# Optimization experiments

Hardware: AMD Instinct MI355X
Metric: run time of the kernel (lower is better)

Reference implementation:

```python
import jax, jax.numpy as jnp
import numpy as np

E = 8        # num_experts
K = 2        # num_experts_per_tok
H = 1024     # hidden_dim
F = 2816     # intermediate_dim
R = 256      # shared-core rank
B, S = 2, 1024


def setup_inputs() -> dict:
    key = jax.random.key(0)
    ks = jax.random.split(key, 12)
    inp = {
        "hidden_states": jax.random.normal(ks[0], (B, S, H), jnp.float32),
        "gate_w": jax.random.normal(ks[1], (H, E), jnp.float32) / np.sqrt(H),
        # gate_proj: hidden -> intermediate, factored W_e = Ug[e] @ Cg @ Vg[e]
        "Ug": jax.random.normal(ks[2], (E, H, R), jnp.float32) / np.sqrt(H),
        "Cg": jax.random.normal(ks[3], (R, R), jnp.float32) / np.sqrt(R),
        "Vg": jax.random.normal(ks[4], (E, R, F), jnp.float32) / np.sqrt(R),
        # up_proj: hidden -> intermediate
        "Uu": jax.random.normal(ks[5], (E, H, R), jnp.float32) / np.sqrt(H),
        "Cu": jax.random.normal(ks[6], (R, R), jnp.float32) / np.sqrt(R),
        "Vu": jax.random.normal(ks[7], (E, R, F), jnp.float32) / np.sqrt(R),
        # down_proj: intermediate -> hidden
        "Ud": jax.random.normal(ks[8], (E, F, R), jnp.float32) / np.sqrt(F),
        "Cd": jax.random.normal(ks[9], (R, R), jnp.float32) / np.sqrt(R),
        "Vd": jax.random.normal(ks[10], (E, R, H), jnp.float32) / np.sqrt(R),
    }
    return inp


def _moe_forward(x, gate_w, Ug, Cg, Vg, Uu, Cu, Vu, Ud, Cd, Vd):
    b, s, h = x.shape
    xf = x.reshape(-1, h)                       # [T, H]
    T = xf.shape[0]
    logits = xf @ gate_w                        # [T, E]
    probs = jax.nn.softmax(logits, axis=-1)
    w, idx = jax.lax.top_k(probs, K)            # [T, K]
    w = w / jnp.sum(w, axis=-1, keepdims=True)
    # dense combine weights: combine[t, e] = sum of renormalized routing
    # weights over top-k slots routed to expert e (scatter-add in torch code)
    combine = jnp.zeros((T, E), xf.dtype).at[jnp.arange(T)[:, None], idx].add(w)
    out = jnp.zeros_like(xf)
    for e in range(E):  # fixed small expert count
        g = (xf @ Ug[e]) @ Cg @ Vg[e]           # [T, F]
        u = (xf @ Uu[e]) @ Cu @ Vu[e]           # [T, F]
        a = jax.nn.silu(g) * u
        y = (a @ Ud[e]) @ Cd @ Vd[e]            # [T, H]
        out = out + combine[:, e:e + 1] * y
    return out.reshape(b, s, h)


def reference(hidden_states, gate_w, Ug, Cg, Vg, Uu, Cu, Vu, Ud, Cd, Vd):
    return _moe_forward(hidden_states, gate_w, Ug, Cg, Vg, Uu, Cu, Vu, Ud, Cd, Vd)
```

## Files before the change

kernel.cpp:

```cpp
#include <hip/hip_runtime.h>
#include <math.h>

constexpr int cE = 8;
constexpr int cH = 1024;
constexpr int cF = 2816;
constexpr int cR = 256;
constexpr int cT = 2048;
constexpr int ROWS = cT * 2;
constexpr int LDA = 40;

using short8  = __attribute__((ext_vector_type(8))) short;
using float4v = __attribute__((ext_vector_type(4))) float;
#define MFMA16 __builtin_amdgcn_mfma_f32_16x16x32_bf16

__device__ __forceinline__ unsigned short f2bf(float f) {
  union { float f; unsigned u; } v; v.f = f;
  unsigned r = v.u + 0x7fffu + ((v.u >> 16) & 1u);
  return (unsigned short)(r >> 16);
}
__device__ __forceinline__ float bf2f(unsigned short s) {
  union { unsigned u; float f; } v; v.u = (unsigned)s << 16; return v.f;
}

__device__ __forceinline__ void store_bf8(unsigned short* dst, float4 a, float4 b) {
  union { unsigned short u[8]; uint4 v; } t;
  t.u[0] = f2bf(a.x); t.u[1] = f2bf(a.y); t.u[2] = f2bf(a.z); t.u[3] = f2bf(a.w);
  t.u[4] = f2bf(b.x); t.u[5] = f2bf(b.y); t.u[6] = f2bf(b.z); t.u[7] = f2bf(b.w);
  *reinterpret_cast<uint4*>(dst) = t.v;
}

__device__ __forceinline__ void gld16(const unsigned short* g, unsigned short* l) {
  __builtin_amdgcn_global_load_lds(
      (const __attribute__((address_space(1))) void*)g,
      (__attribute__((address_space(3))) void*)l, 16, 0, 0);
}

__device__ __forceinline__ void tconv_tile64(
    const float* __restrict__ in, unsigned short* __restrict__ out,
    int P, int Q, int e, int bx, int by, int tid, float (*tile)[65])
{
  const long es = (long)P * Q;
  in += e * es; out += e * es;
  const int c0 = bx * 64, r0 = by * 64;
  const int r = tid >> 4, c4 = (tid & 15) * 4;
#pragma unroll
  for (int p = 0; p < 4; ++p) {
    float4 v = *reinterpret_cast<const float4*>(
        in + (long)(r0 + p * 16 + r) * Q + c0 + c4);
    tile[p * 16 + r][c4 + 0] = v.x; tile[p * 16 + r][c4 + 1] = v.y;
    tile[p * 16 + r][c4 + 2] = v.z; tile[p * 16 + r][c4 + 3] = v.w;
  }
  __syncthreads();
  const int cc = tid >> 4, rr4 = (tid & 15) * 4;
#pragma unroll
  for (int p = 0; p < 4; ++p) {
    ushort4 o;
    o.x = f2bf(tile[rr4 + 0][p * 16 + cc]);
    o.y = f2bf(tile[rr4 + 1][p * 16 + cc]);
    o.z = f2bf(tile[rr4 + 2][p * 16 + cc]);
    o.w = f2bf(tile[rr4 + 3][p * 16 + cc]);
    *reinterpret_cast<ushort4*>(out + (long)(c0 + p * 16 + cc) * P + r0 + rr4) = o;
  }
}

constexpr int TCONV_BLOCKS = 4768;
constexpr int PREP1_BLOCKS = TCONV_BLOCKS + cT / 4;

__global__ __launch_bounds__(256) void k_prep1(
    const float* __restrict__ Cg, unsigned short* __restrict__ CgT,
    const float* __restrict__ Cu, unsigned short* __restrict__ CuT,
    const float* __restrict__ Vd, unsigned short* __restrict__ VdT,
    const float* __restrict__ Vg, unsigned short* __restrict__ vgT,
    const float* __restrict__ Vu, unsigned short* __restrict__ vuT,
    const float* __restrict__ Ud, unsigned short* __restrict__ udT,
    const float* __restrict__ x, const float* __restrict__ gw,
    unsigned short* __restrict__ xb, int* __restrict__ et,
    float* __restrict__ wt)
{
  __shared__ float tile[64][65];
  int b = blockIdx.x;
  const int tid = threadIdx.x;
  if (b < TCONV_BLOCKS) {
    const float* in; unsigned short* out; int P, Q;
    if (b < 16)         { in = Cg; out = CgT; P = 256;  Q = 256;  }
    else if (b < 32)    { b -= 16;    in = Cu; out = CuT; P = 256;  Q = 256;  }
    else if (b < 544)   { b -= 32;    in = Vd; out = VdT; P = 256;  Q = 1024; }
    else if (b < 1952)  { b -= 544;   in = Vg; out = vgT; P = 256;  Q = 2816; }
    else if (b < 3360)  { b -= 1952;  in = Vu; out = vuT; P = 256;  Q = 2816; }
    else                { b -= 3360;  in = Ud; out = udT; P = 2816; Q = 256;  }
    const int tpe = (P / 64) * (Q / 64);
    const int e = b / tpe, rem = b % tpe;
    const int bx = rem % (Q / 64), by = rem / (Q / 64);
    tconv_tile64(in, out, P, Q, e, bx, by, tid, tile);
    return;
  }
  const int wid = tid >> 6, lane = tid & 63;
  const int t = (b - TCONV_BLOCKS) * 4 + wid;
  const float* xr = x + (long)t * cH + lane * 16;
  float4 v0 = *reinterpret_cast<const float4*>(xr);
  float4 v1 = *reinterpret_cast<const float4*>(xr + 4);
  float4 v2 = *reinterpret_cast<const float4*>(xr + 8);
  float4 v3 = *reinterpret_cast<const float4*>(xr + 12);
  store_bf8(xb + (long)t * cH + lane * 16, v0, v1);
  store_bf8(xb + (long)t * cH + lane * 16 + 8, v2, v3);
  float xv[16];
  *reinterpret_cast<float4*>(&xv[0])  = v0;
  *reinterpret_cast<float4*>(&xv[4])  = v1;
  *reinterpret_cast<float4*>(&xv[8])  = v2;
  *reinterpret_cast<float4*>(&xv[12]) = v3;
  const float* g = gw + (long)lane * 16 * cE;
  float l[cE];
#pragma unroll
  for (int e = 0; e < cE; ++e) l[e] = 0.f;
#pragma unroll
  for (int i = 0; i < 16; ++i) {
    float4 ga = *reinterpret_cast<const float4*>(g + i * cE);
    float4 gb = *reinterpret_cast<const float4*>(g + i * cE + 4);
    float xi = xv[i];
    l[0] += xi * ga.x; l[1] += xi * ga.y; l[2] += xi * ga.z; l[3] += xi * ga.w;
    l[4] += xi * gb.x; l[5] += xi * gb.y; l[6] += xi * gb.z; l[7] += xi * gb.w;
  }
#pragma unroll
  for (int m = 1; m < 64; m <<= 1)
#pragma unroll
    for (int e = 0; e < cE; ++e)
      l[e] += __shfl_xor(l[e], m, 64);
  if (lane == 0) {
    int i0 = 0; float m0 = l[0];
#pragma unroll
    for (int e = 1; e < cE; ++e) if (l[e] > m0) { m0 = l[e]; i0 = e; }
    int i1 = -1; float m1 = -1e30f;
#pragma unroll
    for (int e = 0; e < cE; ++e) if (e != i0 && l[e] > m1) { m1 = l[e]; i1 = e; }
    float w0 = 1.f / (1.f + expf(m1 - m0));
    et[t * 2 + 0] = i0;  et[t * 2 + 1] = i1;
    wt[t * 2 + 0] = w0;  wt[t * 2 + 1] = 1.f - w0;
  }
}

__device__ __forceinline__ void foldm_body(
    const unsigned short* __restrict__ A, const float* __restrict__ B,
    unsigned short* __restrict__ D, int ldd, int m0, int n0, int tid,
    unsigned short* As, unsigned short* Bs)
{
  const int sr = tid >> 2, sk = (tid & 3) * 8;
  const unsigned short* a0 = A + (long)(m0 + sr) * 256 + sk;
  const unsigned short* a1 = a0 + (long)64 * 256;
  const float* br = B + (long)(n0 + sr) * 256 + sk;
  uint4 rA0, rA1; float4 rB0, rB1;
  auto load_slice = [&](int k0) {
    rA0 = *reinterpret_cast<const uint4*>(a0 + k0);
    rA1 = *reinterpret_cast<const uint4*>(a1 + k0);
    rB0 = *reinterpret_cast<const float4*>(br + k0);
    rB1 = *reinterpret_cast<const float4*>(br + k0 + 4);
  };
  load_slice(0);
  const int wid = tid >> 6, lane = tid & 63;
  const int wm = (wid >> 1) * 64, wn = (wid & 1) * 32;
  const int fr = lane & 15, fq = lane >> 4;
  float4v zf = {0.f, 0.f, 0.f, 0.f};
  float4v acc[4][2];
#pragma unroll
  for (int i = 0; i < 4; ++i) { acc[i][0] = zf; acc[i][1] = zf; }
  for (int k0 = 0; k0 < 256; k0 += 32) {
    *reinterpret_cast<uint4*>(&As[sr * LDA + sk]) = rA0;
    *reinterpret_cast<uint4*>(&As[(sr + 64) * LDA + sk]) = rA1;
    store_bf8(&Bs[sr * LDA + sk], rB0, rB1);
    if (k0 + 32 < 256) load_slice(k0 + 32);
    __syncthreads();
    short8 af[4], bf[2];
#pragma unroll
    for (int mi = 0; mi < 4; ++mi)
      af[mi] = *reinterpret_cast<const short8*>(&As[(wm + mi * 16 + fr) * LDA + fq * 8]);
#pragma unroll
    for (int nj = 0; nj < 2; ++nj)
      bf[nj] = *reinterpret_cast<const short8*>(&Bs[(wn + nj * 16 + fr) * LDA + fq * 8]);
#pragma unroll
    for (int mi = 0; mi < 4; ++mi)
#pragma unroll
      for (int nj = 0; nj < 2; ++nj)
        acc[mi][nj] = MFMA16(af[mi], bf[nj], acc[mi][nj], 0, 0, 0);
    __syncthreads();
  }
#pragma unroll
  for (int mi = 0; mi < 4; ++mi)
#pragma unroll
    for (int r = 0; r < 4; ++r) {
      int m = m0 + wm + mi * 16 + fq * 4 + r;
#pragma unroll
      for (int nj = 0; nj < 2; ++nj)
        D[(long)m * ldd + n0 + wn + nj * 16 + fr] = f2bf(acc[mi][nj][r]);
    }
}

constexpr int PREP2_BLOCKS = 512 + 256 + 1;
__global__ __launch_bounds__(256, 2) void k_prep2(
    const unsigned short* __restrict__ CgT, const unsigned short* __restrict__ CuT,
    const float* __restrict__ Ug, const float* __restrict__ Uu,
    unsigned short* __restrict__ b1t,
    const unsigned short* __restrict__ VdT, const float* __restrict__ Cd,
    unsigned short* __restrict__ vd2t,
    const int* __restrict__ et, int* __restrict__ rowmap,
    int* __restrict__ tok, int* __restrict__ cnt, int* __restrict__ off)
{
  __shared__ __align__(16) unsigned short As[128 * LDA], Bs[64 * LDA];
  __shared__ int sc_[cE], sp_[cE], so_[cE];
  const int b = blockIdx.x;
  const int tid = threadIdx.x;
  if (b < 512) {
    const int bx = b & 15, by = (b >> 4) & 1, z = b >> 5;
    const int sel = z >> 3, e = z & 7;
    const unsigned short* A = sel ? CuT : CgT;
    const float* B = (sel ? Uu : Ug) + (long)e * cH * cR;
    unsigned short* Dp = b1t + (long)e * 512 * 1024 + (long)sel * 256 * 1024;
    foldm_body(A, B, Dp, cH, by * 128, bx * 64, tid, As, Bs);
  } else if (b < 768) {
    const int b2 = b - 512;
    const int bx = b2 & 3, by = (b2 >> 2) & 7, e = b2 >> 5;
    foldm_body(VdT + (long)e * cH * cR, Cd, vd2t + (long)e * cH * 256, cR,
               by * 128, bx * 64, tid, As, Bs);
  } else {
    if (tid < cE) { sc_[tid] = 0; sp_[tid] = 0; }
    __syncthreads();
    for (int i = tid; i < ROWS; i += 256) atomicAdd(&sc_[et[i]], 1);
    __syncthreads();
    if (tid == 0) {
      int s = 0;
      for (int e = 0; e < cE; ++e) { so_[e] = s; s += sc_[e]; }
    }
    __syncthreads();
    for (int i = tid; i < ROWS; i += 256) {
      int e = et[i];
      int slot = atomicAdd(&sp_[e], 1);
      int cr = so_[e] + slot;
      rowmap[i] = cr;
      tok[cr] = i >> 1;
    }
    if (tid < cE) { cnt[tid] = sc_[tid]; off[tid] = so_[tid]; }
  }
}

__global__ __launch_bounds__(256, 2) void k_t1c(
    const unsigned short* __restrict__ xb, const unsigned short* __restrict__ b1t,
    unsigned short* __restrict__ t1, const int* __restrict__ tok,
    const int* __restrict__ cnt, const int* __restrict__ off)
{
  __shared__ __align__(16) unsigned short As[128 * 64], Bs[64 * 64];
  const int e = blockIdx.z, c = cnt[e], o = off[e];
  const int m0 = blockIdx.y * 128;
  if (m0 >= c) return;
  const int n0 = blockIdx.x * 64;
  const int tid = threadIdx.x;
  const int wid = tid >> 6, lane = tid & 63;
  const int sr8 = lane >> 3, sc = (lane & 7) * 8;
  const unsigned short* gA[4];
#pragma unroll
  for (int j = 0; j < 4; ++j) {
    int row = min(m0 + wid * 32 + j * 8 + sr8, c - 1);
    gA[j] = xb + (long)tok[o + row] * cH + sc;
  }
  const unsigned short* gB = b1t + (long)e * 512 * 1024 +
      (long)(n0 + wid * 16 + sr8) * 1024 + sc;
  unsigned short* lA = As + wid * 32 * 64;
  unsigned short* lB = Bs + wid * 16 * 64;
  const int wm = (wid >> 1) * 64, wn = (wid & 1) * 32;
  const int fr = lane & 15, fq = lane >> 4;
  float4v zf = {0.f, 0.f, 0.f, 0.f};
  float4v acc[4][2];
#pragma unroll
  for (int i = 0; i < 4; ++i) { acc[i][0] = zf; acc[i][1] = zf; }
  for (int k0 = 0; k0 < cH; k0 += 64) {
#pragma unroll
    for (int j = 0; j < 4; ++j) gld16(gA[j] + k0, lA + j * 8 * 64);
    gld16(gB + k0, lB);
    gld16(gB + (long)8 * 1024 + k0, lB + 8 * 64);
    __syncthreads();
#pragma unroll
    for (int ks = 0; ks < 2; ++ks) {
      short8 af[4], bf[2];
#pragma unroll
      for (int mi = 0; mi < 4; ++mi)
        af[mi] = *reinterpret_cast<const short8*>(
            &As[(wm + mi * 16 + fr) * 64 + ks * 32 + fq * 8]);
#pragma unroll
      for (int nj = 0; nj < 2; ++nj)
        bf[nj] = *reinterpret_cast<const short8*>(
            &Bs[(wn + nj * 16 + fr) * 64 + ks * 32 + fq * 8]);
#pragma unroll
      for (int mi = 0; mi < 4; ++mi)
#pragma unroll
        for (int nj = 0; nj < 2; ++nj)
          acc[mi][nj] = MFMA16(af[mi], bf[nj], acc[mi][nj], 0, 0, 0);
    }
    __syncthreads();
  }
#pragma unroll
  for (int mi = 0; mi < 4; ++mi)
#pragma unroll
    for (int r = 0; r < 4; ++r) {
      int row = m0 + wm + mi * 16 + fq * 4 + r;
      if (row < c) {
#pragma unroll
        for (int nj = 0; nj < 2; ++nj)
          t1[(long)(o + row) * 512 + n0 + wn + nj * 16 + fr] = f2bf(acc[mi][nj][r]);
      }
    }
}

__global__ __launch_bounds__(256, 2) void k_act(
    const unsigned short* __restrict__ t1,
    const unsigned short* __restrict__ vgT, const unsigned short* __restrict__ vuT,
    unsigned short* __restrict__ a, const int* __restrict__ cnt,
    const int* __restrict__ off)
{
  __shared__ __align__(16) unsigned short Ag[128 * 64], Au[128 * 64];
  __shared__ __align__(16) unsigned short Bg[64 * 64],  Bu[64 * 64];
  const int e = blockIdx.z, c = cnt[e], o = off[e];
  const int m0 = blockIdx.y * 128;
  if (m0 >= c) return;
  const int n0 = blockIdx.x * 64;
  const int tid = threadIdx.x;
  const int wid = tid >> 6, lane = tid & 63;
  const int sr8 = lane >> 3, sc8 = (lane & 7) * 8;
  const unsigned short* gA[4];
#pragma unroll
  for (int j = 0; j < 4; ++j) {
    int row = o + min(m0 + wid * 32 + j * 8 + sr8, c - 1);
    gA[j] = t1 + (long)row * 512 + sc8;
  }
  const unsigned short* gBg = vgT + (long)e * cF * 256 +
      (long)(n0 + wid * 16 + sr8) * 256 + sc8;
  const unsigned short* gBu = vuT + (long)e * cF * 256 +
      (long)(n0 + wid * 16 + sr8) * 256 + sc8;
  unsigned short* lAg = Ag + wid * 32 * 64;
  unsigned short* lAu = Au + wid * 32 * 64;
  unsigned short* lBg = Bg + wid * 16 * 64;
  unsigned short* lBu = Bu + wid * 16 * 64;
  const int wm = (wid >> 1) * 64, wn = (wid & 1) * 32;
  const int fr = lane & 15, fq = lane >> 4;
  float4v zf = {0.f, 0.f, 0.f, 0.f};
  float4v accg[4][2], accu[4][2];
#pragma unroll
  for (int i = 0; i < 4; ++i) { accg[i][0] = zf; accg[i][1] = zf; accu[i][0] = zf; accu[i][1] = zf; }
  for (int k0 = 0; k0 < 256; k0 += 64) {
#pragma unroll
    for (int j = 0; j < 4; ++j) gld16(gA[j] + k0,       lAg + j * 8 * 64);
#pragma unroll
    for (int j = 0; j < 4; ++j) gld16(gA[j] + 256 + k0, lAu + j * 8 * 64);
#pragma unroll
    for (int j = 0; j < 2; ++j) {
      gld16(gBg + (long)j * 8 * 256 + k0, lBg + j * 8 * 64);
      gld16(gBu + (long)j * 8 * 256 + k0, lBu + j * 8 * 64);
    }
    __syncthreads();
#pragma unroll
    for (int ks = 0; ks < 2; ++ks) {
      short8 ag[4], au[4], bg[2], bu[2];
#pragma unroll
      for (int mi = 0; mi < 4; ++mi) {
        ag[mi] = *reinterpret_cast<const short8*>(
            &Ag[(wm + mi * 16 + fr) * 64 + ks * 32 + fq * 8]);
        au[mi] = *reinterpret_cast<const short8*>(
            &Au[(wm + mi * 16 + fr) * 64 + ks * 32 + fq * 8]);
      }
#pragma unroll
      for (int nj = 0; nj < 2; ++nj) {
        bg[nj] = *reinterpret_cast<const short8*>(
            &Bg[(wn + nj * 16 + fr) * 64 + ks * 32 + fq * 8]);
        bu[nj] = *reinterpret_cast<const short8*>(
            &Bu[(wn + nj * 16 + fr) * 64 + ks * 32 + fq * 8]);
      }
#pragma unroll
      for (int mi = 0; mi < 4; ++mi)
#pragma unroll
        for (int nj = 0; nj < 2; ++nj) {
          accg[mi][nj] = MFMA16(ag[mi], bg[nj], accg[mi][nj], 0, 0, 0);
          accu[mi][nj] = MFMA16(au[mi], bu[nj], accu[mi][nj], 0, 0, 0);
        }
    }
    __syncthreads();
  }
#pragma unroll
  for (int mi = 0; mi < 4; ++mi)
#pragma unroll
    for (int r = 0; r < 4; ++r) {
      int row = m0 + wm + mi * 16 + fq * 4 + r;
      if (row < c) {
#pragma unroll
        for (int nj = 0; nj < 2; ++nj) {
          float g = accg[mi][nj][r];
          float u = accu[mi][nj][r];
          float s = g / (1.f + expf(-g)) * u;
          a[(long)(o + row) * cF + n0 + wn + nj * 16 + fr] = f2bf(s);
        }
      }
    }
}

__global__ __launch_bounds__(256, 2) void k_t3(
    const unsigned short* __restrict__ a, const unsigned short* __restrict__ udT,
    float* __restrict__ t3p, const int* __restrict__ cnt,
    const int* __restrict__ off)
{
  __shared__ __align__(16) unsigned short As[64 * 64], Bs[64 * 64];
  const int e = blockIdx.z, c = cnt[e], o = off[e];
  const int m0 = blockIdx.y * 64;
  if (m0 >= c) return;
  const int n0 = (blockIdx.x & 3) * 64;
  const int ksp = blockIdx.x >> 2;
  const int kbase = ksp * 1408;
  const int tid = threadIdx.x;
  const int wid = tid >> 6, lane = tid & 63;
  const int sr8 = lane >> 3, sc = (lane & 7) * 8;
  const int ra0 = o + min(m0 + wid * 16 + sr8, c - 1);
  const int ra1 = o + min(m0 + wid * 16 + 8 + sr8, c - 1);
  const unsigned short* gA0 = a + (long)ra0 * cF + kbase + sc;
  const unsigned short* gA1 = a + (long)ra1 * cF + kbase + sc;
  const unsigned short* gB  = udT + (long)e * 256 * cF + (long)(n0 + wid * 16 + sr8) * cF + kbase + sc;
  unsigned short* lA = As + wid * 16 * 64;
  unsigned short* lB = Bs + wid * 16 * 64;
  const int wm = (wid >> 1) * 32, wn = (wid & 1) * 32;
  const int fr = lane & 15, fq = lane >> 4;
  float4v zf = {0.f, 0.f, 0.f, 0.f};
  float4v acc[2][2] = {{zf, zf}, {zf, zf}};
  for (int k0 = 0; k0 < 1408; k0 += 64) {
    gld16(gA0 + k0, lA);
    gld16(gA1 + k0, lA + 8 * 64);
    gld16(gB + k0, lB);
    gld16(gB + (long)8 * cF + k0, lB + 8 * 64);
    __syncthreads();
#pragma unroll
    for (int ks = 0; ks < 2; ++ks) {
      short8 af[2], bf[2];
#pragma unroll
      for (int mi = 0; mi < 2; ++mi)
        af[mi] = *reinterpret_cast<const short8*>(
            &As[(wm + mi * 16 + fr) * 64 + ks * 32 + fq * 8]);
#pragma unroll
      for (int nj = 0; nj < 2; ++nj)
        bf[nj] = *reinterpret_cast<const short8*>(
            &Bs[(wn + nj * 16 + fr) * 64 + ks * 32 + fq * 8]);
#pragma unroll
      for (int mi = 0; mi < 2; ++mi)
#pragma unroll
        for (int nj = 0; nj < 2; ++nj)
          acc[mi][nj] = MFMA16(af[mi], bf[nj], acc[mi][nj], 0, 0, 0);
    }
    __syncthreads();
  }
  float* dstbase = t3p + (long)ksp * ROWS * 256;
#pragma unroll
  for (int mi = 0; mi < 2; ++mi)
#pragma unroll
    for (int r = 0; r < 4; ++r) {
      int row = m0 + wm + mi * 16 + fq * 4 + r;
      if (row < c) {
        float* dst = dstbase + (long)(o + row) * 256 + n0 + wn;
#pragma unroll
        for (int nj = 0; nj < 2; ++nj)
          dst[nj * 16 + fr] = acc[mi][nj][r];
      }
    }
}

__global__ __launch_bounds__(256) void k_red2(
    const float* __restrict__ t3p, unsigned short* __restrict__ t3b)
{
  const long psz = (long)ROWS * 256;
  long i = ((long)blockIdx.x * 256 + threadIdx.x) * 8;
  float4 s0 = *reinterpret_cast<const float4*>(t3p + i);
  float4 s1 = *reinterpret_cast<const float4*>(t3p + i + 4);
  float4 a0 = *reinterpret_cast<const float4*>(t3p + psz + i);
  float4 a1 = *reinterpret_cast<const float4*>(t3p + psz + i + 4);
  s0.x += a0.x; s0.y += a0.y; s0.z += a0.z; s0.w += a0.w;
  s1.x += a1.x; s1.y += a1.y; s1.z += a1.z; s1.w += a1.w;
  store_bf8(t3b + i, s0, s1);
}

__global__ __launch_bounds__(256, 2) void k_y(
    const unsigned short* __restrict__ t3b, const unsigned short* __restrict__ vd2t,
    unsigned short* __restrict__ y, const int* __restrict__ cnt,
    const int* __restrict__ off)
{
  __shared__ __align__(16) unsigned short As[128 * 32], Bs[64 * 32];
  const int e = blockIdx.z, c = cnt[e], o = off[e];
  const int m0 = blockIdx.y * 128;
  if (m0 >= c) return;
  const int n0 = blockIdx.x * 64;
  const int tid = threadIdx.x;
  const int wid = tid >> 6, lane = tid & 63;
  const int sr16 = lane >> 2, sc = (lane & 3) * 8;
  const int ra0 = o + min(m0 + wid * 32 + sr16, c - 1);
  const int ra1 = o + min(m0 + wid * 32 + 16 + sr16, c - 1);
  const unsigned short* gA0 = t3b + (long)ra0 * 256 + sc;
  const unsigned short* gA1 = t3b + (long)ra1 * 256 + sc;
  const unsigned short* gB  = vd2t + (long)e * cH * 256 + (long)(n0 + wid * 16 + sr16) * 256 + sc;
  unsigned short* lA = As + wid * 32 * 32;
  unsigned short* lB = Bs + wid * 16 * 32;
  const int wm = (wid >> 1) * 64, wn = (wid & 1) * 32;
  const int fr = lane & 15, fq = lane >> 4;
  float4v zf = {0.f, 0.f, 0.f, 0.f};
  float4v acc[4][2];
#pragma unroll
  for (int i = 0; i < 4; ++i) { acc[i][0] = zf; acc[i][1] = zf; }
  for (int k0 = 0; k0 < 256; k0 += 32) {
    gld16(gA0 + k0, lA);
    gld16(gA1 + k0, lA + 16 * 32);
    gld16(gB + k0, lB);
    __syncthreads();
    short8 af[4], bf[2];
#pragma unroll
    for (int mi = 0; mi < 4; ++mi)
      af[mi] = *reinterpret_cast<const short8*>(&As[(wm + mi * 16 + fr) * 32 + fq * 8]);
#pragma unroll
    for (int nj = 0; nj < 2; ++nj)
      bf[nj] = *reinterpret_cast<const short8*>(&Bs[(wn + nj * 16 + fr) * 32 + fq * 8]);
#pragma unroll
    for (int mi = 0; mi < 4; ++mi)
#pragma unroll
      for (int nj = 0; nj < 2; ++nj)
        acc[mi][nj] = MFMA16(af[mi], bf[nj], acc[mi][nj], 0, 0, 0);
    __syncthreads();
  }
#pragma unroll
  for (int mi = 0; mi < 4; ++mi)
#pragma unroll
    for (int r = 0; r < 4; ++r) {
      int row = m0 + wm + mi * 16 + fq * 4 + r;
      if (row < c) {
#pragma unroll
        for (int nj = 0; nj < 2; ++nj)
          y[(long)(o + row) * cH + n0 + wn + nj * 16 + fr] = f2bf(acc[mi][nj][r]);
      }
    }
}

__global__ __launch_bounds__(256) void k_combine(
    const unsigned short* __restrict__ y, const float* __restrict__ wt,
    const int* __restrict__ rowmap, float* __restrict__ out)
{
  const int tid = threadIdx.x;
  const int t = blockIdx.x * 2 + (tid >> 7);
  const int h = (tid & 127) * 8;
  const int r0 = rowmap[2 * t], r1 = rowmap[2 * t + 1];
  const float w0 = wt[2 * t], w1 = wt[2 * t + 1];
  union { uint4 v; unsigned short s[8]; } ua, ub;
  ua.v = *reinterpret_cast<const uint4*>(y + (long)r0 * cH + h);
  ub.v = *reinterpret_cast<const uint4*>(y + (long)r1 * cH + h);
  float o[8];
#pragma unroll
  for (int i = 0; i < 8; ++i)
    o[i] = w0 * bf2f(ua.s[i]) + w1 * bf2f(ub.s[i]);
  float* dst = out + (long)t * cH + h;
  *reinterpret_cast<float4*>(dst)     = make_float4(o[0], o[1], o[2], o[3]);
  *reinterpret_cast<float4*>(dst + 4) = make_float4(o[4], o[5], o[6], o[7]);
}

extern "C" void kernel_launch(void* const* d_in, const int* in_sizes, int n_in,
                              void* d_out, int out_size, void* d_ws, size_t ws_size,
                              hipStream_t stream)
{
  const float* x  = (const float*)d_in[0];
  const float* gw = (const float*)d_in[1];
  const float* Ug = (const float*)d_in[2];
  const float* Cg = (const float*)d_in[3];
  const float* Vg = (const float*)d_in[4];
  const float* Uu = (const float*)d_in[5];
  const float* Cu = (const float*)d_in[6];
  const float* Vu = (const float*)d_in[7];
  const float* Ud = (const float*)d_in[8];
  const float* Cd = (const float*)d_in[9];
  const float* Vd = (const float*)d_in[10];
  float* out = (float*)d_out;

  char* w = (char*)d_ws;
  unsigned short* vgT = (unsigned short*)w;
  float*          t3p = (float*)w;
  unsigned short* t3b = (unsigned short*)(w + (long)2 * ROWS * 256 * 4);
  w += (long)cE * cF * 256 * 2;
  unsigned short* b1t = (unsigned short*)w;  w += (long)cE * 512 * 1024 * 2;
  unsigned short* vd2t = (unsigned short*)w; w += (long)cE * cH * 256 * 2;
  unsigned short* vuT = (unsigned short*)w;
  unsigned short* yb  = (unsigned short*)w;  w += (long)cE * cF * 256 * 2;
  unsigned short* udT = (unsigned short*)w;  w += (long)cE * 256 * cF * 2;
  unsigned short* VdT = (unsigned short*)w;  w += (long)cE * cH * 256 * 2;
  unsigned short* xb  = (unsigned short*)w;  w += (long)cT * cH * 2;
  unsigned short* CgT = (unsigned short*)w;  w += (long)cR * cR * 2;
  unsigned short* CuT = (unsigned short*)w;  w += (long)cR * cR * 2;
  unsigned short* t1  = (unsigned short*)w;  w += (long)ROWS * 512 * 2;
  unsigned short* ab  = (unsigned short*)w;  w += (long)ROWS * cF * 2;
  float* wt   = (float*)w; w += ROWS * 4;
  int* et     = (int*)w; w += ROWS * 4;
  int* rowmap = (int*)w; w += ROWS * 4;
  int* tok    = (int*)w; w += ROWS * 4;
  int* cnt = (int*)w; w += cE * 4;
  int* off = (int*)w; w += cE * 4;

  k_prep1<<<dim3(PREP1_BLOCKS), dim3(256), 0, stream>>>(
      Cg, CgT, Cu, CuT, Vd, VdT, Vg, vgT, Vu, vuT, Ud, udT, x, gw, xb, et, wt);
  k_prep2<<<dim3(PREP2_BLOCKS), dim3(256), 0, stream>>>(
      CgT, CuT, Ug, Uu, b1t, VdT, Cd, vd2t, et, rowmap, tok, cnt, off);
  k_t1c<<<dim3(8, cT / 128, cE), dim3(256), 0, stream>>>(xb, b1t, t1, tok, cnt, off);
  k_act<<<dim3(cF / 64, cT / 128, cE), dim3(256), 0, stream>>>(t1, vgT, vuT, ab, cnt, off);
  k_t3<<<dim3(8, cT / 64, cE), dim3(256), 0, stream>>>(ab, udT, t3p, cnt, off);
  k_red2<<<dim3(ROWS * 256 / (256 * 8)), dim3(256), 0, stream>>>(t3p, t3b);
  k_y<<<dim3(cH / 64, cT / 128, cE), dim3(256), 0, stream>>>(t3b, vd2t, yb, cnt, off);
  k_combine<<<dim3(cT / 2), dim3(256), 0, stream>>>(yb, wt, rowmap, out);
}
```

Baseline: 304.8 us.

## Double-buffer LDS in all grouped GEMM kernels and widen split-K for down-proj

Converts the k_t1c, k_act, k_t3 and k_y GEMM loops to double-buffered shared memory, issuing the next tile's loads before computing the current one. This drops one barrier per iteration and overlaps global loads with MFMA work. k_t3 now splits K four ways instead of two, with an XOR swizzle on its LDS layout to cut bank conflicts. The reduction kernel sums four partials, and launch bounds are raised to ask for more resident blocks. The risks are more register and LDS pressure and more partial-sum traffic through the workspace.

Result: faster. 279.5 us (-8.3%).

```diff
diff --git a/kernel.cpp b/kernel.cpp
--- a/kernel.cpp
+++ b/kernel.cpp
@@ -240,12 +240,12 @@
   }
 }
 
-__global__ __launch_bounds__(256, 2) void k_t1c(
+__global__ __launch_bounds__(256, 3) void k_t1c(
     const unsigned short* __restrict__ xb, const unsigned short* __restrict__ b1t,
     unsigned short* __restrict__ t1, const int* __restrict__ tok,
     const int* __restrict__ cnt, const int* __restrict__ off)
 {
-  __shared__ __align__(16) unsigned short As[128 * 64], Bs[64 * 64];
+  __shared__ __align__(16) unsigned short As[2][128 * 64], Bs[2][64 * 64];
   const int e = blockIdx.z, c = cnt[e], o = off[e];
   const int m0 = blockIdx.y * 128;
   if (m0 >= c) return;
@@ -261,31 +261,36 @@
   }
   const unsigned short* gB = b1t + (long)e * 512 * 1024 +
       (long)(n0 + wid * 16 + sr8) * 1024 + sc;
-  unsigned short* lA = As + wid * 32 * 64;
-  unsigned short* lB = Bs + wid * 16 * 64;
+  const int lA = wid * 32 * 64;
+  const int lB = wid * 16 * 64;
+  auto STAGE = [&](int k0, int buf) {
+#pragma unroll
+    for (int j = 0; j < 4; ++j) gld16(gA[j] + k0, &As[buf][lA + j * 8 * 64]);
+    gld16(gB + k0, &Bs[buf][lB]);
+    gld16(gB + (long)8 * 1024 + k0, &Bs[buf][lB + 8 * 64]);
+  };
   const int wm = (wid >> 1) * 64, wn = (wid & 1) * 32;
   const int fr = lane & 15, fq = lane >> 4;
   float4v zf = {0.f, 0.f, 0.f, 0.f};
   float4v acc[4][2];
 #pragma unroll
   for (int i = 0; i < 4; ++i) { acc[i][0] = zf; acc[i][1] = zf; }
-  for (int k0 = 0; k0 < cH; k0 += 64) {
-#pragma unroll
-    for (int j = 0; j < 4; ++j) gld16(gA[j] + k0, lA + j * 8 * 64);
-    gld16(gB + k0, lB);
-    gld16(gB + (long)8 * 1024 + k0, lB + 8 * 64);
-    __syncthreads();
+  STAGE(0, 0);
+  __syncthreads();
+  for (int t = 0; t < 16; ++t) {
+    const int cur = t & 1;
+    if (t < 15) STAGE((t + 1) * 64, cur ^ 1);
 #pragma unroll
     for (int ks = 0; ks < 2; ++ks) {
       short8 af[4], bf[2];
 #pragma unroll
       for (int mi = 0; mi < 4; ++mi)
         af[mi] = *reinterpret_cast<const short8*>(
-            &As[(wm + mi * 16 + fr) * 64 + ks * 32 + fq * 8]);
+            &As[cur][(wm + mi * 16 + fr) * 64 + ks * 32 + fq * 8]);
 #pragma unroll
       for (int nj = 0; nj < 2; ++nj)
         bf[nj] = *reinterpret_cast<const short8*>(
-            &Bs[(wn + nj * 16 + fr) * 64 + ks * 32 + fq * 8]);
+            &Bs[cur][(wn + nj * 16 + fr) * 64 + ks * 32 + fq * 8]);
 #pragma unroll
       for (int mi = 0; mi < 4; ++mi)
 #pragma unroll
@@ -307,77 +312,66 @@
     }
 }
 
-__global__ __launch_bounds__(256, 2) void k_act(
+__global__ __launch_bounds__(256, 3) void k_act(
     const unsigned short* __restrict__ t1,
     const unsigned short* __restrict__ vgT, const unsigned short* __restrict__ vuT,
     unsigned short* __restrict__ a, const int* __restrict__ cnt,
     const int* __restrict__ off)
 {
-  __shared__ __align__(16) unsigned short Ag[128 * 64], Au[128 * 64];
-  __shared__ __align__(16) unsigned short Bg[64 * 64],  Bu[64 * 64];
+  __shared__ __align__(16) unsigned short Ag[2][128 * 32], Au[2][128 * 32];
+  __shared__ __align__(16) unsigned short Bg[2][64 * 32],  Bu[2][64 * 32];
   const int e = blockIdx.z, c = cnt[e], o = off[e];
   const int m0 = blockIdx.y * 128;
   if (m0 >= c) return;
   const int n0 = blockIdx.x * 64;
   const int tid = threadIdx.x;
   const int wid = tid >> 6, lane = tid & 63;
-  const int sr8 = lane >> 3, sc8 = (lane & 7) * 8;
-  const unsigned short* gA[4];
-#pragma unroll
-  for (int j = 0; j < 4; ++j) {
-    int row = o + min(m0 + wid * 32 + j * 8 + sr8, c - 1);
-    gA[j] = t1 + (long)row * 512 + sc8;
-  }
-  const unsigned short* gBg = vgT + (long)e * cF * 256 +
-      (long)(n0 + wid * 16 + sr8) * 256 + sc8;
-  const unsigned short* gBu = vuT + (long)e * cF * 256 +
-      (long)(n0 + wid * 16 + sr8) * 256 + sc8;
-  unsigned short* lAg = Ag + wid * 32 * 64;
-  unsigned short* lAu = Au + wid * 32 * 64;
-  unsigned short* lBg = Bg + wid * 16 * 64;
-  unsigned short* lBu = Bu + wid * 16 * 64;
+  const int sr16 = lane >> 2, sc = (lane & 3) * 8;
+  const int ra0 = o + min(m0 + wid * 32 + sr16, c - 1);
+  const int ra1 = o + min(m0 + wid * 32 + 16 + sr16, c - 1);
+  const unsigned short* gAg0 = t1 + (long)ra0 * 512 + sc;
+  const unsigned short* gAg1 = t1 + (long)ra1 * 512 + sc;
+  const unsigned short* gBg = vgT + (long)e * cF * 256 + (long)(n0 + wid * 16 + sr16) * 256 + sc;
+  const unsigned short* gBu = vuT + (long)e * cF * 256 + (long)(n0 + wid * 16 + sr16) * 256 + sc;
+  const int lA = wid * 32 * 32;
+  const int lB = wid * 16 * 32;
+  auto STAGE = [&](int k0, int buf) {
+    gld16(gAg0 + k0, &Ag[buf][lA]);
+    gld16(gAg1 + k0, &Ag[buf][lA + 16 * 32]);
+    gld16(gAg0 + 256 + k0, &Au[buf][lA]);
+    gld16(gAg1 + 256 + k0, &Au[buf][lA + 16 * 32]);
+    gld16(gBg + k0, &Bg[buf][lB]);
+    gld16(gBu + k0, &Bu[buf][lB]);
+  };
   const int wm = (wid >> 1) * 64, wn = (wid & 1) * 32;
   const int fr = lane & 15, fq = lane >> 4;
   float4v zf = {0.f, 0.f, 0.f, 0.f};
   float4v accg[4][2], accu[4][2];
 #pragma unroll
   for (int i = 0; i < 4; ++i) { accg[i][0] = zf; accg[i][1] = zf; accu[i][0] = zf; accu[i][1] = zf; }
-  for (int k0 = 0; k0 < 256; k0 += 64) {
-#pragma unroll
-    for (int j = 0; j < 4; ++j) gld16(gA[j] + k0,       lAg + j * 8 * 64);
-#pragma unroll
-    for (int j = 0; j < 4; ++j) gld16(gA[j] + 256 + k0, lAu + j * 8 * 64);
-#pragma unroll
-    for (int j = 0; j < 2; ++j) {
-      gld16(gBg + (long)j * 8 * 256 + k0, lBg + j * 8 * 64);
-      gld16(gBu + (long)j * 8 * 256 + k0, lBu + j * 8 * 64);
-    }
-    __syncthreads();
-#pragma unroll
-    for (int ks = 0; ks < 2; ++ks) {
-      short8 ag[4], au[4], bg[2], bu[2];
-#pragma unroll
-      for (int mi = 0; mi < 4; ++mi) {
-        ag[mi] = *reinterpret_cast<const short8*>(
-            &Ag[(wm + mi * 16 + fr) * 64 + ks * 32 + fq * 8]);
-        au[mi] = *reinterpret_cast<const short8*>(
-            &Au[(wm + mi * 16 + fr) * 64 + ks * 32 + fq * 8]);
+  STAGE(0, 0);
+  __syncthreads();
+  for (int t = 0; t < 8; ++t) {
+    const int cur = t & 1;
+    if (t < 7) STAGE((t + 1) * 32, cur ^ 1);
+    short8 ag[4], au[4], bg[2], bu[2];
+#pragma unroll
+    for (int mi = 0; mi < 4; ++mi) {
+      ag[mi] = *reinterpret_cast<const short8*>(&Ag[cur][(wm + mi * 16 + fr) * 32 + fq * 8]);
+      au[mi] = *reinterpret_cast<const short8*>(&Au[cur][(wm + mi * 16 + fr) * 32 + fq * 8]);
+    }
+#pragma unroll
+    for (int nj = 0; nj < 2; ++nj) {
+      bg[nj] = *reinterpret_cast<const short8*>(&Bg[cur][(wn + nj * 16 + fr) * 32 + fq * 8]);
+      bu[nj] = *reinterpret_cast<const short8*>(&Bu[cur][(wn + nj * 16 + fr) * 32 + fq * 8]);
+    }
+#pragma unroll
+    for (int mi = 0; mi < 4; ++mi)
+#pragma unroll
+      for (int nj = 0; nj < 2; ++nj) {
+        accg[mi][nj] = MFMA16(ag[mi], bg[nj], accg[mi][nj], 0, 0, 0);
+        accu[mi][nj] = MFMA16(au[mi], bu[nj], accu[mi][nj], 0, 0, 0);
       }
-#pragma unroll
-      for (int nj = 0; nj < 2; ++nj) {
-        bg[nj] = *reinterpret_cast<const short8*>(
-            &Bg[(wn + nj * 16 + fr) * 64 + ks * 32 + fq * 8]);
-        bu[nj] = *reinterpret_cast<const short8*>(
-            &Bu[(wn + nj * 16 + fr) * 64 + ks * 32 + fq * 8]);
-      }
-#pragma unroll
-      for (int mi = 0; mi < 4; ++mi)
-#pragma unroll
-        for (int nj = 0; nj < 2; ++nj) {
-          accg[mi][nj] = MFMA16(ag[mi], bg[nj], accg[mi][nj], 0, 0, 0);
-          accu[mi][nj] = MFMA16(au[mi], bu[nj], accu[mi][nj], 0, 0, 0);
-        }
-    }
     __syncthreads();
   }
 #pragma unroll
@@ -397,49 +391,56 @@
     }
 }
 
-__global__ __launch_bounds__(256, 2) void k_t3(
+__global__ __launch_bounds__(256, 4) void k_t3(
     const unsigned short* __restrict__ a, const unsigned short* __restrict__ udT,
     float* __restrict__ t3p, const int* __restrict__ cnt,
     const int* __restrict__ off)
 {
-  __shared__ __align__(16) unsigned short As[64 * 64], Bs[64 * 64];
+  __shared__ __align__(16) unsigned short As[2][64 * 64], Bs[2][64 * 64];
   const int e = blockIdx.z, c = cnt[e], o = off[e];
   const int m0 = blockIdx.y * 64;
   if (m0 >= c) return;
   const int n0 = (blockIdx.x & 3) * 64;
   const int ksp = blockIdx.x >> 2;
-  const int kbase = ksp * 1408;
+  const int kbase = ksp * 704;
   const int tid = threadIdx.x;
   const int wid = tid >> 6, lane = tid & 63;
-  const int sr8 = lane >> 3, sc = (lane & 7) * 8;
+  const int sr8 = lane >> 3;
+  const int scs = ((lane & 7) ^ sr8) * 8;
   const int ra0 = o + min(m0 + wid * 16 + sr8, c - 1);
   const int ra1 = o + min(m0 + wid * 16 + 8 + sr8, c - 1);
-  const unsigned short* gA0 = a + (long)ra0 * cF + kbase + sc;
-  const unsigned short* gA1 = a + (long)ra1 * cF + kbase + sc;
-  const unsigned short* gB  = udT + (long)e * 256 * cF + (long)(n0 + wid * 16 + sr8) * cF + kbase + sc;
-  unsigned short* lA = As + wid * 16 * 64;
-  unsigned short* lB = Bs + wid * 16 * 64;
+  const unsigned short* gA0 = a + (long)ra0 * cF + kbase + scs;
+  const unsigned short* gA1 = a + (long)ra1 * cF + kbase + scs;
+  const unsigned short* gB  = udT + (long)e * 256 * cF +
+      (long)(n0 + wid * 16 + sr8) * cF + kbase + scs;
+  const int lofs = wid * 16 * 64;
+  auto STAGE = [&](int k0, int buf) {
+    gld16(gA0 + k0, &As[buf][lofs]);
+    gld16(gA1 + k0, &As[buf][lofs + 8 * 64]);
+    gld16(gB + k0, &Bs[buf][lofs]);
+    gld16(gB + (long)8 * cF + k0, &Bs[buf][lofs + 8 * 64]);
+  };
   const int wm = (wid >> 1) * 32, wn = (wid & 1) * 32;
   const int fr = lane & 15, fq = lane >> 4;
+  const int swz = (fr & 7) * 8;
   float4v zf = {0.f, 0.f, 0.f, 0.f};
   float4v acc[2][2] = {{zf, zf}, {zf, zf}};
-  for (int k0 = 0; k0 < 1408; k0 += 64) {
-    gld16(gA0 + k0, lA);
-    gld16(gA1 + k0, lA + 8 * 64);
-    gld16(gB + k0, lB);
-    gld16(gB + (long)8 * cF + k0, lB + 8 * 64);
-    __syncthreads();
+  STAGE(0, 0);
+  __syncthreads();
+  for (int t = 0; t < 11; ++t) {
+    const int cur = t & 1;
+    if (t < 10) STAGE((t + 1) * 64, cur ^ 1);
 #pragma unroll
     for (int ks = 0; ks < 2; ++ks) {
       short8 af[2], bf[2];
 #pragma unroll
       for (int mi = 0; mi < 2; ++mi)
         af[mi] = *reinterpret_cast<const short8*>(
-            &As[(wm + mi * 16 + fr) * 64 + ks * 32 + fq * 8]);
+            &As[cur][(wm + mi * 16 + fr) * 64 + ((ks * 32 + fq * 8) ^ swz)]);
 #pragma unroll
       for (int nj = 0; nj < 2; ++nj)
         bf[nj] = *reinterpret_cast<const short8*>(
-            &Bs[(wn + nj * 16 + fr) * 64 + ks * 32 + fq * 8]);
+            &Bs[cur][(wn + nj * 16 + fr) * 64 + ((ks * 32 + fq * 8) ^ swz)]);
 #pragma unroll
       for (int mi = 0; mi < 2; ++mi)
 #pragma unroll
@@ -463,26 +464,29 @@
     }
 }
 
-__global__ __launch_bounds__(256) void k_red2(
+__global__ __launch_bounds__(256) void k_red(
     const float* __restrict__ t3p, unsigned short* __restrict__ t3b)
 {
   const long psz = (long)ROWS * 256;
   long i = ((long)blockIdx.x * 256 + threadIdx.x) * 8;
   float4 s0 = *reinterpret_cast<const float4*>(t3p + i);
   float4 s1 = *reinterpret_cast<const float4*>(t3p + i + 4);
-  float4 a0 = *reinterpret_cast<const float4*>(t3p + psz + i);
-  float4 a1 = *reinterpret_cast<const float4*>(t3p + psz + i + 4);
-  s0.x += a0.x; s0.y += a0.y; s0.z += a0.z; s0.w += a0.w;
-  s1.x += a1.x; s1.y += a1.y; s1.z += a1.z; s1.w += a1.w;
+#pragma unroll
+  for (int q = 1; q < 4; ++q) {
+    float4 a0 = *reinterpret_cast<const float4*>(t3p + q * psz + i);
+    float4 a1 = *reinterpret_cast<const float4*>(t3p + q * psz + i + 4);
+    s0.x += a0.x; s0.y += a0.y; s0.z += a0.z; s0.w += a0.w;
+    s1.x += a1.x; s1.y += a1.y; s1.z += a1.z; s1.w += a1.w;
+  }
   store_bf8(t3b + i, s0, s1);
 }
 
-__global__ __launch_bounds__(256, 2) void k_y(
+__global__ __launch_bounds__(256, 4) void k_y(
     const unsigned short* __restrict__ t3b, const unsigned short* __restrict__ vd2t,
     unsigned short* __restrict__ y, const int* __restrict__ cnt,
     const int* __restrict__ off)
 {
-  __shared__ __align__(16) unsigned short As[128 * 32], Bs[64 * 32];
+  __shared__ __align__(16) unsigned short As[2][128 * 32], Bs[2][64 * 32];
   const int e = blockIdx.z, c = cnt[e], o = off[e];
   const int m0 = blockIdx.y * 128;
   if (m0 >= c) return;
@@ -495,26 +499,31 @@
   const unsigned short* gA0 = t3b + (long)ra0 * 256 + sc;
   const unsigned short* gA1 = t3b + (long)ra1 * 256 + sc;
   const unsigned short* gB  = vd2t + (long)e * cH * 256 + (long)(n0 + wid * 16 + sr16) * 256 + sc;
-  unsigned short* lA = As + wid * 32 * 32;
-  unsigned short* lB = Bs + wid * 16 * 32;
+  const int lA = wid * 32 * 32;
+  const int lB = wid * 16 * 32;
+  auto STAGE = [&](int k0, int buf) {
+    gld16(gA0 + k0, &As[buf][lA]);
+    gld16(gA1 + k0, &As[buf][lA + 16 * 32]);
+    gld16(gB + k0, &Bs[buf][lB]);
+  };
   const int wm = (wid >> 1) * 64, wn = (wid & 1) * 32;
   const int fr = lane & 15, fq = lane >> 4;
   float4v zf = {0.f, 0.f, 0.f, 0.f};
   float4v acc[4][2];
 #pragma unroll
   for (int i = 0; i < 4; ++i) { acc[i][0] = zf; acc[i][1] = zf; }
-  for (int k0 = 0; k0 < 256; k0 += 32) {
-    gld16(gA0 + k0, lA);
-    gld16(gA1 + k0, lA + 16 * 32);
-    gld16(gB + k0, lB);
-    __syncthreads();
+  STAGE(0, 0);
+  __syncthreads();
+  for (int t = 0; t < 8; ++t) {
+    const int cur = t & 1;
+    if (t < 7) STAGE((t + 1) * 32, cur ^ 1);
     short8 af[4], bf[2];
 #pragma unroll
     for (int mi = 0; mi < 4; ++mi)
-      af[mi] = *reinterpret_cast<const short8*>(&As[(wm + mi * 16 + fr) * 32 + fq * 8]);
+      af[mi] = *reinterpret_cast<const short8*>(&As[cur][(wm + mi * 16 + fr) * 32 + fq * 8]);
 #pragma unroll
     for (int nj = 0; nj < 2; ++nj)
-      bf[nj] = *reinterpret_cast<const short8*>(&Bs[(wn + nj * 16 + fr) * 32 + fq * 8]);
+      bf[nj] = *reinterpret_cast<const short8*>(&Bs[cur][(wn + nj * 16 + fr) * 32 + fq * 8]);
 #pragma unroll
     for (int mi = 0; mi < 4; ++mi)
 #pragma unroll
@@ -576,7 +585,7 @@
   char* w = (char*)d_ws;
   unsigned short* vgT = (unsigned short*)w;
   float*          t3p = (float*)w;
-  unsigned short* t3b = (unsigned short*)(w + (long)2 * ROWS * 256 * 4);
+  unsigned short* t3b = (unsigned short*)(w + (long)4 * ROWS * 256 * 4);
   w += (long)cE * cF * 256 * 2;
   unsigned short* b1t = (unsigned short*)w;  w += (long)cE * 512 * 1024 * 2;
   unsigned short* vd2t = (unsigned short*)w; w += (long)cE * cH * 256 * 2;
@@ -602,8 +611,8 @@
       CgT, CuT, Ug, Uu, b1t, VdT, Cd, vd2t, et, rowmap, tok, cnt, off);
   k_t1c<<<dim3(8, cT / 128, cE), dim3(256), 0, stream>>>(xb, b1t, t1, tok, cnt, off);
   k_act<<<dim3(cF / 64, cT / 128, cE), dim3(256), 0, stream>>>(t1, vgT, vuT, ab, cnt, off);
-  k_t3<<<dim3(8, cT / 64, cE), dim3(256), 0, stream>>>(ab, udT, t3p, cnt, off);
-  k_red2<<<dim3(ROWS * 256 / (256 * 8)), dim3(256), 0, stream>>>(t3p, t3b);
+  k_t3<<<dim3(16, cT / 64, cE), dim3(256), 0, stream>>>(ab, udT, t3p, cnt, off);
+  k_red<<<dim3(ROWS * 256 / (256 * 8)), dim3(256), 0, stream>>>(t3p, t3b);
   k_y<<<dim3(cH / 64, cT / 128, cE), dim3(256), 0, stream>>>(t3b, vd2t, yb, cnt, off);
   k_combine<<<dim3(cT / 2), dim3(256), 0, stream>>>(yb, wt, rowmap, out);
 }
```
